# Kernel optimization log

Hardware: AMD Instinct MI355X
Metric: run time of the kernel (lower is better)

## Reference

```python
import jax, jax.numpy as jnp
import numpy as np

B, N, S, K = 8, 4096, 256, 128   # clouds, points/cloud, FPS samples (num_vote_test), neighbor cap
R = 0.2                           # ball-query radius
M = 45                            # FoldingNet grid side -> 45*45 = 2025 grid points


def _fps(pos):
    """Deterministic farthest point sampling of S points from pos [N,3] (start at index 0)."""
    n = pos.shape[0]
    big = jnp.finfo(pos.dtype).max

    def step(carry, _):
        mind, last = carry
        d = jnp.sum((pos - pos[last]) ** 2, axis=-1)
        mind = jnp.minimum(mind, d)
        nxt = jnp.argmax(mind).astype(jnp.int32)
        return (mind, nxt), nxt

    init = (jnp.full((n,), big, pos.dtype), jnp.int32(0))
    _, rest = jax.lax.scan(step, init, None, length=S - 1)
    return jnp.concatenate([jnp.zeros((1,), jnp.int32), rest])


def _forward(pos, Wt, bt, Wc1, bc1, Wc2, bc2, Wc3, bc3, We1, be1, We2, be2,
             Wf11, bf11, Wf12, bf12, Wf13, bf13, Wf21, bf21, Wf22, bf22, Wf23, bf23):
    lrelu = jax.nn.leaky_relu  # slope 0.01, matches torch LeakyReLU default
    # transformer: mlp([3,64]) -- BatchNorm at eval with default stats is identity
    x = lrelu(pos @ Wt + bt)                                  # [B,N,64]
    # FPS per cloud
    idx = jax.vmap(_fps)(pos)                                  # [B,S]
    new_pos = jnp.take_along_axis(pos, idx[..., None], axis=1)  # [B,S,3]
    # radius ball query: first K in-ball neighbors by index order (torch_cluster semantics)
    d2 = jnp.sum((new_pos[:, :, None, :] - pos[:, None, :, :]) ** 2, -1)  # [B,S,N]
    inball = d2 <= R * R
    keep = inball & (jnp.cumsum(inball, axis=-1) <= K)
    order = jnp.where(keep, jnp.arange(N)[None, None, :], N)
    nidx = jnp.sort(order, axis=-1)[..., :K]                   # [B,S,K]
    valid = nidx < N
    nsafe = jnp.minimum(nidx, N - 1)
    gather = jax.vmap(lambda a, i: a[i])
    xj = gather(x, nsafe)                                      # [B,S,K,64]
    pj = gather(pos, nsafe)                                    # [B,S,K,3]
    # PointConv: mlp(cat[x_j, pos_j - pos_i]) with max aggregation
    feat = jnp.concatenate([xj, pj - new_pos[:, :, None, :]], -1)  # [B,S,K,67]
    h = lrelu(feat @ Wc1 + bc1)
    h = lrelu(h @ Wc2 + bc2)
    h = lrelu(h @ Wc3 + bc3)                                   # [B,S,K,512]
    neg = jnp.finfo(h.dtype).min
    agg = jnp.max(jnp.where(valid[..., None], h, neg), axis=2)  # [B,S,512]
    # encoder mlp([515, 512, 2*bottleneck], last=True)
    e = lrelu(jnp.concatenate([agg, new_pos], -1) @ We1 + be1)
    e = e @ We2 + be2                                          # [B,S,2*bottleneck]
    mean, logvar = jnp.split(e, 2, axis=-1)
    std = jnp.exp(0.5 * logvar)
    # feature_selection (eval, rand=False): all S votes contribute; vote aggregation
    z = jnp.sum(mean / std, axis=1) / jnp.sum(1.0 / std, axis=1)  # [B,bottleneck]
    # FoldingNet decoder: 45x45 grid in [-0.3,0.3]^2, conv1x1 == last-dim linear
    g1 = np.linspace(-0.3, 0.3, M, dtype=np.float32)
    mg = np.meshgrid(g1, g1)
    grid = jnp.asarray(np.stack([mg[0].reshape(-1), mg[1].reshape(-1)], -1))  # [M*M,2]
    G = M * M
    code = jnp.broadcast_to(z[:, None, :], (z.shape[0], G, z.shape[1]))
    gb = jnp.broadcast_to(grid[None], (z.shape[0], G, 2))
    f = jnp.concatenate([code, gb], -1)                        # [B,G,bottleneck+2]
    f = jax.nn.relu(f @ Wf11 + bf11)
    f = jax.nn.relu(f @ Wf12 + bf12)
    f = f @ Wf13 + bf13                                        # [B,G,3]
    f2 = jnp.concatenate([code, f], -1)                        # [B,G,bottleneck+3]
    f2 = jax.nn.relu(f2 @ Wf21 + bf21)
    f2 = jax.nn.relu(f2 @ Wf22 + bf22)
    return f2 @ Wf23 + bf23                                    # [B,G,3]


_PARAM_SHAPES = [
    ("Wt", (3, 64)), ("bt", (64,)),
    ("Wc1", (67, 64)), ("bc1", (64,)),
    ("Wc2", (64, 128)), ("bc2", (128,)),
    ("Wc3", (128, 512)), ("bc3", (512,)),
    ("We1", (515, 512)), ("be1", (512,)),
    ("We2", (512, 2048)), ("be2", (2048,)),
    ("Wf11", (1026, 512)), ("bf11", (512,)),
    ("Wf12", (512, 512)), ("bf12", (512,)),
    ("Wf13", (512, 3)), ("bf13", (3,)),
    ("Wf21", (1027, 512)), ("bf21", (512,)),
    ("Wf22", (512, 512)), ("bf22", (512,)),
    ("Wf23", (512, 3)), ("bf23", (3,)),
]


def setup_inputs() -> dict:
    key = jax.random.key(0)
    inp = {"pos": jax.random.uniform(key, (B, N, 3), jnp.float32)}
    for i, (nm, sh) in enumerate(_PARAM_SHAPES):
        k = jax.random.fold_in(key, i + 1)
        fan_in = sh[0]
        inp[nm] = jax.random.normal(k, sh, jnp.float32) / np.sqrt(fan_in)
    return inp


def reference(pos, Wt, bt, Wc1, bc1, Wc2, bc2, Wc3, bc3, We1, be1, We2, be2,
              Wf11, bf11, Wf12, bf12, Wf13, bf13, Wf21, bf21, Wf22, bf22, Wf23, bf23):
    return _forward(pos, Wt, bt, Wc1, bc1, Wc2, bc2, Wc3, bc3, We1, be1, We2, be2,
                    Wf11, bf11, Wf12, bf12, Wf13, bf13, Wf21, bf21, Wf22, bf22, Wf23, bf23)
```

## Files before the change

### kernel.cpp

```cpp
#include <hip/hip_runtime.h>
#include <math.h>

#define BATCH 8
#define NPTS 4096
#define SSAMP 256
#define KNBR 128
#define GGRID 2025

typedef __attribute__((ext_vector_type(8))) short bf16x8;
typedef __attribute__((ext_vector_type(8))) unsigned short u16x8;
typedef __attribute__((ext_vector_type(4))) float f32x4;
#define MFMA16(a, b, c) __builtin_amdgcn_mfma_f32_16x16x32_bf16((a), (b), (c), 0, 0, 0)

__device__ __forceinline__ float lrelu01(float v) { return v > 0.f ? v : 0.01f * v; }
__device__ __forceinline__ unsigned short f2bf(float f) {
    unsigned u = __float_as_uint(f);
    unsigned r = (u + 0x7FFFu + ((u >> 16) & 1u)) >> 16;
    return (unsigned short)r;
}
__device__ __forceinline__ unsigned long long umax64(unsigned long long a, unsigned long long b) {
    return a > b ? a : b;
}
__device__ __forceinline__ void spin_ge(const int* p, int target) {
    while (__hip_atomic_load(p, __ATOMIC_RELAXED, __HIP_MEMORY_SCOPE_AGENT) < target)
        __builtin_amdgcn_s_sleep(16);
}
__device__ __forceinline__ float aload(const float* p) {
    return __hip_atomic_load((float*)p, __ATOMIC_RELAXED, __HIP_MEMORY_SCOPE_AGENT);
}
__device__ __forceinline__ void astore(float* p, float v) {
    __hip_atomic_store(p, v, __ATOMIC_RELAXED, __HIP_MEMORY_SCOPE_AGENT);
}

__global__ void preconv_kernel(const float* __restrict__ Wc1, const float* __restrict__ Wc2,
                               const float* __restrict__ Wc3, const float* __restrict__ We1,
                               const float* __restrict__ We2, const float* __restrict__ Wf12,
                               const float* __restrict__ Wf22,
                               unsigned short* __restrict__ W1T, unsigned short* __restrict__ W2T,
                               unsigned short* __restrict__ W3T, unsigned short* __restrict__ We1T,
                               unsigned short* __restrict__ We2T, unsigned short* __restrict__ Wf12T,
                               unsigned short* __restrict__ Wf22T) {
    int o = blockIdx.x * 256 + threadIdx.x;
    const int S1 = 6144, S2 = 8192, S3 = 65536, S4 = 294912, S5 = 1048576, S6 = 262144;
    if (o < S1) { int n = o / 96, k = o - n * 96; W1T[o] = f2bf(k < 67 ? Wc1[k * 64 + n] : 0.f); return; }
    o -= S1;
    if (o < S2) { int n = o >> 6, k = o & 63; W2T[o] = f2bf(Wc2[k * 128 + n]); return; }
    o -= S2;
    if (o < S3) { int n = o >> 7, k = o & 127; W3T[o] = f2bf(Wc3[k * 512 + n]); return; }
    o -= S3;
    if (o < S4) { int n = o / 576, k = o - n * 576; We1T[o] = f2bf(k < 515 ? We1[k * 512 + n] : 0.f); return; }
    o -= S4;
    if (o < S5) {
        int np = o >> 9, k = o & 511;
        int src = (np & 1) ? 1024 + (np >> 1) : (np >> 1);
        We2T[o] = f2bf(We2[(size_t)k * 2048 + src]);
        return;
    }
    o -= S5;
    if (o < S6) { int n = o >> 9, k = o & 511; Wf12T[o] = f2bf(Wf12[k * 512 + n]); return; }
    o -= S6;
    { int n = o >> 9, k = o & 511; Wf22T[o] = f2bf(Wf22[k * 512 + n]); }
}

__global__ void __launch_bounds__(256, 3) stage1_kernel(
    const float* __restrict__ pos, float* __restrict__ newpos, int* __restrict__ prog,
    const float* __restrict__ Wt, const float* __restrict__ bt,
    const unsigned short* __restrict__ W1T, const unsigned short* __restrict__ W2T,
    const unsigned short* __restrict__ W3T,
    const float* __restrict__ bc1, const float* __restrict__ bc2, const float* __restrict__ bc3,
    unsigned short* __restrict__ encin) {
    __shared__ __align__(16) unsigned char smem[53760];
    int blk = blockIdx.x, t = threadIdx.x;
    int wave = t >> 6, lane = t & 63;

    if (blk < 8) {
        float* pxs = (float*)smem;
        float* pys = (float*)(smem + 16384);
        float* pzs = (float*)(smem + 32768);
        float* npb = (float*)(smem + 49152);
        unsigned long long* rk = (unsigned long long*)(smem + 52224);
        int b = blk;
        const float* P = pos + (size_t)b * NPTS * 3;
        float* np = newpos + (size_t)b * SSAMP * 3;
        float px[16], py[16], pz[16], mind[16];
#pragma unroll
        for (int j = 0; j < 16; ++j) {
            int n = t + 256 * j;
            float X = P[n * 3 + 0], Y = P[n * 3 + 1], Z = P[n * 3 + 2];
            px[j] = X; py[j] = Y; pz[j] = Z;
            pxs[n] = X; pys[n] = Y; pzs[n] = Z;
            mind[j] = 3.402823466e+38f;
        }
        float cx = P[0], cy = P[1], cz = P[2];
        if (t == 0) { npb[0] = cx; npb[1] = cy; npb[2] = cz; }
        __syncthreads();
        for (int s = 1; s < SSAMP; ++s) {
            int p = s & 1;
            unsigned long long k[16];
#pragma unroll
            for (int j = 0; j < 16; ++j) {
                float dx = __fsub_rn(px[j], cx), dy = __fsub_rn(py[j], cy), dz = __fsub_rn(pz[j], cz);
                float d = __fadd_rn(__fadd_rn(__fmul_rn(dx, dx), __fmul_rn(dy, dy)), __fmul_rn(dz, dz));
                mind[j] = fminf(mind[j], d);
                k[j] = ((unsigned long long)__float_as_uint(mind[j]) << 32)
                     | (unsigned)~(unsigned)(t + 256 * j);
            }
#pragma unroll
            for (int st = 8; st > 0; st >>= 1)
#pragma unroll
                for (int j = 0; j < st; ++j) k[j] = umax64(k[j], k[j + st]);
            unsigned long long key = k[0];
            {
                unsigned long long a = __shfl_xor(key, 1, 64);
                unsigned long long b2 = __shfl_xor(key, 2, 64);
                unsigned long long c = __shfl_xor(key, 3, 64);
                key = umax64(umax64(key, a), umax64(b2, c));
                a = __shfl_xor(key, 4, 64);
                b2 = __shfl_xor(key, 8, 64);
                c = __shfl_xor(key, 12, 64);
                key = umax64(umax64(key, a), umax64(b2, c));
                a = __shfl_xor(key, 16, 64);
                b2 = __shfl_xor(key, 32, 64);
                c = __shfl_xor(key, 48, 64);
                key = umax64(umax64(key, a), umax64(b2, c));
            }
            if (lane == 0) rk[p * 4 + wave] = key;
            __syncthreads();
            unsigned long long k0 = rk[p * 4 + 0], k1 = rk[p * 4 + 1];
            unsigned long long k2 = rk[p * 4 + 2], k3 = rk[p * 4 + 3];
            unsigned long long bk = umax64(umax64(k0, k1), umax64(k2, k3));
            int nx = (int)(~(unsigned)(bk & 0xFFFFFFFFull));
            cx = pxs[nx]; cy = pys[nx]; cz = pzs[nx];
            if (t == 0) {
                npb[s * 3 + 0] = cx;
                npb[s * 3 + 1] = cy;
                npb[s * 3 + 2] = cz;
            }
            if ((s & 7) == 7) {
                if (t < 24) astore(&np[(s - 7) * 3 + t], npb[(s - 7) * 3 + t]);
                if (t == 0 && s >= 15)
                    __hip_atomic_store(&prog[b], s - 8, __ATOMIC_RELAXED, __HIP_MEMORY_SCOPE_AGENT);
            }
        }
        __syncthreads();
        if (t == 0)
            __hip_atomic_store(&prog[b], 255, __ATOMIC_RELAXED, __HIP_MEMORY_SCOPE_AGENT);
        return;
    }

    unsigned short* featl = (unsigned short*)smem;
    unsigned short* h2    = (unsigned short*)smem;
    unsigned short* h1    = (unsigned short*)(smem + 34816);
    float* mred = (float*)(smem + 34816);
    int*   vld  = (int*)(smem + 53248);
    int*   wl   = (int*)smem;
    int*   cnt  = (int*)(smem + 2048);
    float* wtb  = (float*)(smem + 26624);

    int cons = blk - 8;
    int s = cons >> 3, b = cons & 7;
    int bs = b * 256 + s;
    int quad = lane >> 4, l16 = lane & 15;

    if (t == 0) spin_ge(&prog[b], s);
    __syncthreads();
    float q0 = aload(&newpos[(size_t)bs * 3 + 0]);
    float q1 = aload(&newpos[(size_t)bs * 3 + 1]);
    float q2 = aload(&newpos[(size_t)bs * 3 + 2]);

    const float* P = pos + (size_t)b * NPTS * 3;
    {
        int base = 0;
        for (int c = 0; c < 16 && base < KNBR; ++c) {
            int n = wave * 1024 + c * 64 + lane;
            float dx = __fsub_rn(P[n * 3 + 0], q0);
            float dy = __fsub_rn(P[n * 3 + 1], q1);
            float dz = __fsub_rn(P[n * 3 + 2], q2);
            float d2 = __fadd_rn(__fadd_rn(__fmul_rn(dx, dx), __fmul_rn(dy, dy)), __fmul_rn(dz, dz));
            bool in = (d2 <= 0.04f);
            unsigned long long mask = __ballot(in);
            if (in) {
                int p = base + __popcll(mask & ((1ull << lane) - 1ull));
                if (p < KNBR) wl[wave * 128 + p] = n;
            }
            base += __popcll(mask);
        }
        if (lane == 0) cnt[wave] = base < KNBR ? base : KNBR;
    }
    __syncthreads();
    {
        int c0 = cnt[0], c1 = cnt[1], c2 = cnt[2], c3 = cnt[3];
        if (t < 128) {
            int idx = -1, r = t;
            if (r < c0) idx = wl[r];
            else {
                r -= c0;
                if (r < c1) idx = wl[128 + r];
                else {
                    r -= c1;
                    if (r < c2) idx = wl[256 + r];
                    else { r -= c2; if (r < c3) idx = wl[384 + r]; }
                }
            }
            vld[t] = idx;
        }
        if (t < 192) wtb[t] = Wt[t];
        else wtb[t] = bt[t - 192];
    }
    __syncthreads();

    int vbits = 0;
#pragma unroll
    for (int i = 0; i < 2; ++i)
#pragma unroll
        for (int reg = 0; reg < 4; ++reg)
            if (vld[(2 * wave + i) * 16 + quad * 4 + reg] >= 0) vbits |= 1 << (i * 4 + reg);

    {
        int sr = t >> 1, sh = t & 1;
        int n = vld[sr];
        int ns = n < 0 ? 0 : n;
        const float* pp = pos + ((size_t)b * NPTS + ns) * 3;
        float p0 = pp[0], p1 = pp[1], p2 = pp[2];
        unsigned short* frow = &featl[sr * 104];
        u16x8 z8 = {0, 0, 0, 0, 0, 0, 0, 0};
        if (n >= 0) {
#pragma unroll
            for (int g = 0; g < 4; ++g) {
                u16x8 v8;
#pragma unroll
                for (int e = 0; e < 8; ++e) {
                    int c = sh * 32 + g * 8 + e;
                    float v = fmaf(p2, wtb[128 + c], fmaf(p1, wtb[64 + c], fmaf(p0, wtb[c], wtb[192 + c])));
                    v8[e] = (unsigned short)f2bf(lrelu01(v));
                }
                *(u16x8*)&frow[sh * 32 + g * 8] = v8;
            }
        } else {
#pragma unroll
            for (int g = 0; g < 4; ++g) *(u16x8*)&frow[sh * 32 + g * 8] = z8;
        }
        if (sh == 1) {
            u16x8 dv = z8;
            if (n >= 0) {
                dv[0] = (unsigned short)f2bf(__fsub_rn(p0, q0));
                dv[1] = (unsigned short)f2bf(__fsub_rn(p1, q1));
                dv[2] = (unsigned short)f2bf(__fsub_rn(p2, q2));
            }
            *(u16x8*)&frow[64] = dv;
            *(u16x8*)&frow[72] = z8;
            *(u16x8*)&frow[80] = z8;
            *(u16x8*)&frow[88] = z8;
        }
    }
    __syncthreads();

    {
        f32x4 acc[2][4];
#pragma unroll
        for (int i = 0; i < 2; ++i)
#pragma unroll
            for (int nt = 0; nt < 4; ++nt) acc[i][nt] = (f32x4){0.f, 0.f, 0.f, 0.f};
#pragma unroll
        for (int ks = 0; ks < 3; ++ks) {
            bf16x8 afr[2];
#pragma unroll
            for (int i = 0; i < 2; ++i)
                afr[i] = *(const bf16x8*)&featl[((2 * wave + i) * 16 + l16) * 104 + ks * 32 + quad * 8];
#pragma unroll
            for (int nt = 0; nt < 4; ++nt) {
                bf16x8 bfr = *(const bf16x8*)(W1T + (nt * 16 + l16) * 96 + ks * 32 + quad * 8);
                acc[0][nt] = MFMA16(afr[0], bfr, acc[0][nt]);
                acc[1][nt] = MFMA16(afr[1], bfr, acc[1][nt]);
            }
        }
#pragma unroll
        for (int i = 0; i < 2; ++i)
#pragma unroll
            for (int nt = 0; nt < 4; ++nt) {
                int col = nt * 16 + l16;
                float bias = bc1[col];
#pragma unroll
                for (int reg = 0; reg < 4; ++reg) {
                    int row = (2 * wave + i) * 16 + quad * 4 + reg;
                    h1[row * 72 + col] = f2bf(lrelu01(acc[i][nt][reg] + bias));
                }
            }
    }
    __syncthreads();

    {
        f32x4 acc[2][8];
#pragma unroll
        for (int i = 0; i < 2; ++i)
#pragma unroll
            for (int nt = 0; nt < 8; ++nt) acc[i][nt] = (f32x4){0.f, 0.f, 0.f, 0.f};
#pragma unroll
        for (int ks = 0; ks < 2; ++ks) {
            bf16x8 afr[2];
#pragma unroll
            for (int i = 0; i < 2; ++i)
                afr[i] = *(const bf16x8*)&h1[((2 * wave + i) * 16 + l16) * 72 + ks * 32 + quad * 8];
#pragma unroll
            for (int nt = 0; nt < 8; ++nt) {
                bf16x8 bfr = *(const bf16x8*)(W2T + (nt * 16 + l16) * 64 + ks * 32 + quad * 8);
                acc[0][nt] = MFMA16(afr[0], bfr, acc[0][nt]);
                acc[1][nt] = MFMA16(afr[1], bfr, acc[1][nt]);
            }
        }
        __syncthreads();
#pragma unroll
        for (int i = 0; i < 2; ++i)
#pragma unroll
            for (int nt = 0; nt < 8; ++nt) {
                int col = nt * 16 + l16;
                float bias = bc2[col];
#pragma unroll
                for (int reg = 0; reg < 4; ++reg) {
                    int row = (2 * wave + i) * 16 + quad * 4 + reg;
                    h2[row * 136 + col] = f2bf(lrelu01(acc[i][nt][reg] + bias));
                }
            }
    }
    __syncthreads();

    for (int c3 = 0; c3 < 4; ++c3) {
        f32x4 acc[2][8];
#pragma unroll
        for (int i = 0; i < 2; ++i)
#pragma unroll
            for (int nt = 0; nt < 8; ++nt) acc[i][nt] = (f32x4){0.f, 0.f, 0.f, 0.f};
#pragma unroll
        for (int ks = 0; ks < 4; ++ks) {
            bf16x8 afr[2];
#pragma unroll
            for (int i = 0; i < 2; ++i)
                afr[i] = *(const bf16x8*)&h2[((2 * wave + i) * 16 + l16) * 136 + ks * 32 + quad * 8];
#pragma unroll
            for (int nt = 0; nt < 8; ++nt) {
                bf16x8 bfr = *(const bf16x8*)(W3T + ((size_t)((c3 * 8 + nt) * 16 + l16)) * 128 + ks * 32 + quad * 8);
                acc[0][nt] = MFMA16(afr[0], bfr, acc[0][nt]);
                acc[1][nt] = MFMA16(afr[1], bfr, acc[1][nt]);
            }
        }
#pragma unroll
        for (int nt = 0; nt < 8; ++nt) {
            float vmax = -3.402823466e+38f;
#pragma unroll
            for (int i = 0; i < 2; ++i)
#pragma unroll
                for (int reg = 0; reg < 4; ++reg)
                    if (vbits & (1 << (i * 4 + reg))) vmax = fmaxf(vmax, acc[i][nt][reg]);
            vmax = fmaxf(vmax, __shfl_xor(vmax, 16));
            vmax = fmaxf(vmax, __shfl_xor(vmax, 32));
            if (lane < 16) mred[wave * 512 + (c3 * 8 + nt) * 16 + l16] = vmax;
        }
    }
    __syncthreads();
    unsigned short* erow = encin + (size_t)bs * 576;
    for (int c = t; c < 576; c += 256) {
        unsigned short v;
        if (c < 512) {
            float m4 = fmaxf(fmaxf(mred[c], mred[512 + c]), fmaxf(mred[1024 + c], mred[1536 + c]));
            v = f2bf(lrelu01(m4 + bc3[c]));
        } else if (c < 515) {
            v = f2bf(c == 512 ? q0 : (c == 513 ? q1 : q2));
        } else v = 0;
        erow[c] = v;
    }
}

__global__ void __launch_bounds__(256, 2) tail_kernel(
    const unsigned short* __restrict__ encinh, const unsigned short* __restrict__ We1T,
    const float* __restrict__ be1, unsigned short* __restrict__ e1h,
    const unsigned short* __restrict__ We2T, const float* __restrict__ be2,
    float* __restrict__ zacc, int* __restrict__ cnts,
    const float* __restrict__ Wf11, const float* __restrict__ bf11,
    const float* __restrict__ Wf21, const float* __restrict__ bf21,
    float* __restrict__ u1, float* __restrict__ u2,
    const unsigned short* __restrict__ Wf12T, const float* __restrict__ bf12,
    const float* __restrict__ Wf13, const float* __restrict__ bf13,
    const unsigned short* __restrict__ Wf22T, const float* __restrict__ bf22,
    const float* __restrict__ Wf23, const float* __restrict__ bf23,
    float* __restrict__ pts, float* __restrict__ outv) {
    __shared__ __align__(16) unsigned char smem[40960];
    int blk = blockIdx.x, t = threadIdx.x;
    int wave = t >> 6, lane = t & 63, quad = lane >> 4, l16 = lane & 15;

    if (blk < 320) {
        unsigned short* As = (unsigned short*)smem;
        bool is_e1 = blk < 64;
        int rb, cb;
        const unsigned short* A;
        const unsigned short* BT;
        int Ka;
        if (is_e1) { rb = blk >> 2; cb = blk & 3; A = encinh; BT = We1T; Ka = 576; }
        else {
            int j = blk - 64; rb = j >> 4; cb = j & 15; A = e1h; BT = We2T; Ka = 512;
            if (t == 0) spin_ge(&cnts[rb], 4);
            __syncthreads();
            __threadfence();
        }
        int row0 = rb * 128, col0 = cb * 128;
        f32x4 acc[2][8];
#pragma unroll
        for (int i = 0; i < 2; ++i)
#pragma unroll
            for (int nt = 0; nt < 8; ++nt) acc[i][nt] = (f32x4){0.f, 0.f, 0.f, 0.f};
        int nk = Ka >> 6;
        int sr = t >> 1, sh = t & 1;
        const unsigned short* Arow = A + (size_t)(row0 + sr) * Ka + sh * 32;
        for (int ks = 0; ks < nk; ++ks) {
            u16x8 av[4];
#pragma unroll
            for (int j = 0; j < 4; ++j) av[j] = *(const u16x8*)(Arow + ks * 64 + j * 8);
            __syncthreads();
#pragma unroll
            for (int j = 0; j < 4; ++j) *(u16x8*)&As[sr * 72 + sh * 32 + j * 8] = av[j];
            __syncthreads();
#pragma unroll
            for (int ks2 = 0; ks2 < 2; ++ks2) {
                bf16x8 afr0 = *(const bf16x8*)&As[((2 * wave) * 16 + l16) * 72 + ks2 * 32 + quad * 8];
                bf16x8 afr1 = *(const bf16x8*)&As[((2 * wave + 1) * 16 + l16) * 72 + ks2 * 32 + quad * 8];
#pragma unroll
                for (int nt = 0; nt < 8; ++nt) {
                    bf16x8 bfr = *(const bf16x8*)(BT + (size_t)(col0 + nt * 16 + l16) * Ka + ks * 64 + ks2 * 32 + quad * 8);
                    acc[0][nt] = MFMA16(afr0, bfr, acc[0][nt]);
                    acc[1][nt] = MFMA16(afr1, bfr, acc[1][nt]);
                }
            }
        }
        if (is_e1) {
#pragma unroll
            for (int i = 0; i < 2; ++i)
#pragma unroll
                for (int nt = 0; nt < 8; ++nt) {
                    int col = col0 + nt * 16 + l16;
                    float bv = be1[col];
#pragma unroll
                    for (int reg = 0; reg < 4; ++reg) {
                        int row = row0 + (2 * wave + i) * 16 + quad * 4 + reg;
                        e1h[(size_t)row * 512 + col] = f2bf(lrelu01(acc[i][nt][reg] + bv));
                    }
                }
            __syncthreads();
            if (t == 0) { __threadfence(); atomicAdd(&cnts[rb], 1); }
        } else {
            int b = row0 >> 8;
#pragma unroll
            for (int nt = 0; nt < 8; ++nt) {
                int colp = col0 + nt * 16 + l16;
                int c2 = colp >> 1;
                int srcc = (colp & 1) ? 1024 + c2 : c2;
                float bv = be2[srcc];
                float num = 0.f, den = 0.f;
#pragma unroll
                for (int i = 0; i < 2; ++i)
#pragma unroll
                    for (int reg = 0; reg < 4; ++reg) {
                        float val = acc[i][nt][reg] + bv;
                        float par = __shfl_xor(val, 1, 64);
                        float d = expf(-0.5f * par);
                        num += val * d;
                        den += d;
                    }
                num += __shfl_xor(num, 16, 64); den += __shfl_xor(den, 16, 64);
                num += __shfl_xor(num, 32, 64); den += __shfl_xor(den, 32, 64);
                if (quad == 0 && !(l16 & 1)) {
                    atomicAdd(&zacc[((b << 10) + c2) * 2 + 0], num);
                    atomicAdd(&zacc[((b << 10) + c2) * 2 + 1], den);
                }
            }
            __syncthreads();
            if (t == 0) atomicAdd(&cnts[16], 1);
        }
        return;
    }

    if (blk < 336) {
        float* zt = (float*)smem;
        float* red = (float*)(smem + 32768);
        int j = blk - 320;
        int dec = j >> 3, cb = j & 7;
        const float* W = dec ? Wf21 : Wf11;
        const float* bias = dec ? bf21 : bf11;
        float* u = dec ? u2 : u1;
        if (t == 0) spin_ge(&cnts[16], 256);
        __syncthreads();
#pragma unroll
        for (int i = 0; i < 32; ++i) {
            int o = t + i * 256;
            float num = aload(&zacc[o * 2 + 0]);
            float den = aload(&zacc[o * 2 + 1]);
            zt[(o & 1023) * 8 + (o >> 10)] = num / den;
        }
        __syncthreads();
        int c64 = t & 63, kc = t >> 6;
        int co = cb * 64 + c64;
        float acc[8];
#pragma unroll
        for (int r = 0; r < 8; ++r) acc[r] = 0.f;
        for (int i = 0; i < 256; ++i) {
            int ci = kc * 256 + i;
            float w = W[(size_t)ci * 512 + co];
            const float4* zp = (const float4*)&zt[ci * 8];
            float4 z0 = zp[0], z1 = zp[1];
            acc[0] = fmaf(z0.x, w, acc[0]); acc[1] = fmaf(z0.y, w, acc[1]);
            acc[2] = fmaf(z0.z, w, acc[2]); acc[3] = fmaf(z0.w, w, acc[3]);
            acc[4] = fmaf(z1.x, w, acc[4]); acc[5] = fmaf(z1.y, w, acc[5]);
            acc[6] = fmaf(z1.z, w, acc[6]); acc[7] = fmaf(z1.w, w, acc[7]);
        }
#pragma unroll
        for (int r = 0; r < 8; ++r) red[(kc * 64 + c64) * 8 + r] = acc[r];
        __syncthreads();
        if (kc == 0) {
#pragma unroll
            for (int r = 0; r < 8; ++r) {
                float v = red[(0 * 64 + c64) * 8 + r] + red[(1 * 64 + c64) * 8 + r]
                        + red[(2 * 64 + c64) * 8 + r] + red[(3 * 64 + c64) * 8 + r] + bias[co];
                astore(&u[r * 512 + co], v);
            }
        }
        __syncthreads();
        if (t == 0) atomicAdd(&cnts[17 + dec], 1);
        return;
    }

    {
        unsigned short* As = (unsigned short*)smem;
        float* sW = (float*)(smem + 18432);
        float* sU = (float*)(smem + 24576);
        float* sP = (float*)(smem + 28672);
        float* sB = (float*)(smem + 30208);
        float* sRC = (float*)(smem + 30720);
        int dec = blk < 844 ? 0 : 1;
        int idx0 = blk - (dec ? 844 : 336);
        int j = idx0 >> 2, cc = idx0 & 3;
        const float* u = dec ? u2 : u1;
        const float* Wfold = dec ? Wf21 : Wf11;
        int nExtra = dec ? 3 : 2;
        const unsigned short* WT = dec ? Wf22T : Wf12T;
        const float* bmid = dec ? bf22 : bf12;
        const float* wout = dec ? Wf23 : Wf13;
        const float* bout = dec ? bf23 : bf13;
        float* ov = dec ? outv : pts;
        int row0 = j * 128, col0 = cc * 128;
        int b0 = row0 / 2025;

        for (int idx = t; idx < 1536; idx += 256) {
            int r = idx >> 9, c = idx & 511;
            sW[r * 512 + c] = (r < nExtra) ? Wfold[(size_t)(1024 + r) * 512 + c] : 0.f;
        }
        for (int idx = t; idx < 384; idx += 256) sP[idx] = wout[col0 * 3 + idx];
        if (t < 128) sB[t] = bmid[col0 + t];
        if (dec == 0 && t < 128) {
            int rg = row0 + t; if (rg > 16199) rg = 16199;
            int b = rg / 2025, g = rg - b * 2025;
            int i = g / 45, jj = g - i * 45;
            sRC[t * 4 + 0] = (jj == 44) ? 0.3f : (float)(-0.3 + jj * (0.6 / 44.0));
            sRC[t * 4 + 1] = (i == 44) ? 0.3f : (float)(-0.3 + i * (0.6 / 44.0));
            sRC[t * 4 + 2] = 0.f;
            sRC[t * 4 + 3] = __int_as_float(b - b0);
        }

        if (t == 0) {
            spin_ge(&cnts[17 + dec], 8);
            if (dec) spin_ge(&cnts[20 + j], 4);
        }
        __syncthreads();

        for (int idx = t; idx < 1024; idx += 256) {
            int rb = idx >> 9;
            int bb = b0 + rb; if (bb > 7) bb = 7;
            sU[rb * 512 + (idx & 511)] = aload(&u[bb * 512 + (idx & 511)]);
        }
        if (dec == 1 && t < 128) {
            int rg = row0 + t; if (rg > 16199) rg = 16199;
            int b = rg / 2025;
            sRC[t * 4 + 0] = aload(&pts[rg * 3 + 0]);
            sRC[t * 4 + 1] = aload(&pts[rg * 3 + 1]);
            sRC[t * 4 + 2] = aload(&pts[rg * 3 + 2]);
            sRC[t * 4 + 3] = __int_as_float(b - b0);
        }
        __syncthreads();

        float proj[2][4][3];
#pragma unroll
        for (int i = 0; i < 2; ++i)
#pragma unroll
            for (int r = 0; r < 4; ++r) { proj[i][r][0] = 0.f; proj[i][r][1] = 0.f; proj[i][r][2] = 0.f; }

        int sr = t >> 1, sh = t & 1;
        float4 rc = *(const float4*)&sRC[sr * 4];
        int ubi = __float_as_int(rc.w);
        const float* up = sU + ubi * 512;
        f32x4 acc[2][8];
#pragma unroll
        for (int i = 0; i < 2; ++i)
#pragma unroll
            for (int nt = 0; nt < 8; ++nt) acc[i][nt] = (f32x4){0.f, 0.f, 0.f, 0.f};
        for (int ks = 0; ks < 8; ++ks) {
            __syncthreads();
            {
                int cbase = ks * 64 + sh * 32;
                const float4* w0p = (const float4*)&sW[cbase];
                const float4* w1p = (const float4*)&sW[512 + cbase];
                const float4* w2p = (const float4*)&sW[1024 + cbase];
                const float4* uup = (const float4*)&up[cbase];
#pragma unroll
                for (int g4 = 0; g4 < 8; ++g4) {
                    float4 w0 = w0p[g4], w1 = w1p[g4], w2 = w2p[g4], uu = uup[g4];
                    float v0 = fmaf(rc.z, w2.x, fmaf(rc.y, w1.x, fmaf(rc.x, w0.x, uu.x)));
                    float v1 = fmaf(rc.z, w2.y, fmaf(rc.y, w1.y, fmaf(rc.x, w0.y, uu.y)));
                    float v2 = fmaf(rc.z, w2.z, fmaf(rc.y, w1.z, fmaf(rc.x, w0.z, uu.z)));
                    float v3 = fmaf(rc.z, w2.w, fmaf(rc.y, w1.w, fmaf(rc.x, w0.w, uu.w)));
                    uint2 pk;
                    pk.x = (unsigned)f2bf(fmaxf(v0, 0.f)) | ((unsigned)f2bf(fmaxf(v1, 0.f)) << 16);
                    pk.y = (unsigned)f2bf(fmaxf(v2, 0.f)) | ((unsigned)f2bf(fmaxf(v3, 0.f)) << 16);
                    *(uint2*)&As[sr * 72 + sh * 32 + g4 * 4] = pk;
                }
            }
            __syncthreads();
#pragma unroll
            for (int ks2 = 0; ks2 < 2; ++ks2) {
                bf16x8 afr0 = *(const bf16x8*)&As[((2 * wave) * 16 + l16) * 72 + ks2 * 32 + quad * 8];
                bf16x8 afr1 = *(const bf16x8*)&As[((2 * wave + 1) * 16 + l16) * 72 + ks2 * 32 + quad * 8];
#pragma unroll
                for (int nt = 0; nt < 8; ++nt) {
                    bf16x8 bfr = *(const bf16x8*)(WT + (size_t)(col0 + nt * 16 + l16) * 512 + ks * 64 + ks2 * 32 + quad * 8);
                    acc[0][nt] = MFMA16(afr0, bfr, acc[0][nt]);
                    acc[1][nt] = MFMA16(afr1, bfr, acc[1][nt]);
                }
            }
        }
#pragma unroll
        for (int i = 0; i < 2; ++i)
#pragma unroll
            for (int nt = 0; nt < 8; ++nt) {
                int lc = nt * 16 + l16;
                float bv = sB[lc];
                float w0 = sP[lc * 3 + 0], w1 = sP[lc * 3 + 1], w2 = sP[lc * 3 + 2];
#pragma unroll
                for (int reg = 0; reg < 4; ++reg) {
                    float h = fmaxf(acc[i][nt][reg] + bv, 0.f);
                    proj[i][reg][0] = fmaf(h, w0, proj[i][reg][0]);
                    proj[i][reg][1] = fmaf(h, w1, proj[i][reg][1]);
                    proj[i][reg][2] = fmaf(h, w2, proj[i][reg][2]);
                }
            }
        float o0 = (cc == 0) ? bout[0] : 0.f;
        float o1 = (cc == 0) ? bout[1] : 0.f;
        float o2 = (cc == 0) ? bout[2] : 0.f;
#pragma unroll
        for (int i = 0; i < 2; ++i)
#pragma unroll
            for (int reg = 0; reg < 4; ++reg) {
                float p0 = proj[i][reg][0], p1 = proj[i][reg][1], p2 = proj[i][reg][2];
#pragma unroll
                for (int m = 1; m < 16; m <<= 1) {
                    p0 += __shfl_xor(p0, m, 64);
                    p1 += __shfl_xor(p1, m, 64);
                    p2 += __shfl_xor(p2, m, 64);
                }
                if (l16 == 0) {
                    int row = row0 + (2 * wave + i) * 16 + quad * 4 + reg;
                    if (row < 16200) {
                        atomicAdd(&ov[row * 3 + 0], p0 + o0);
                        atomicAdd(&ov[row * 3 + 1], p1 + o1);
                        atomicAdd(&ov[row * 3 + 2], p2 + o2);
                    }
                }
            }
        if (dec == 0) {
            __syncthreads();
            if (t == 0) atomicAdd(&cnts[20 + j], 1);
        }
    }
}

extern "C" void kernel_launch(void* const* d_in, const int* in_sizes, int n_in,
                              void* d_out, int out_size, void* d_ws, size_t ws_size,
                              hipStream_t stream) {
    const float* pos  = (const float*)d_in[0];
    const float* Wt   = (const float*)d_in[1];
    const float* bt   = (const float*)d_in[2];
    const float* Wc1  = (const float*)d_in[3];
    const float* bc1  = (const float*)d_in[4];
    const float* Wc2  = (const float*)d_in[5];
    const float* bc2  = (const float*)d_in[6];
    const float* Wc3  = (const float*)d_in[7];
    const float* bc3  = (const float*)d_in[8];
    const float* We1  = (const float*)d_in[9];
    const float* be1  = (const float*)d_in[10];
    const float* We2  = (const float*)d_in[11];
    const float* be2  = (const float*)d_in[12];
    const float* Wf11 = (const float*)d_in[13];
    const float* bf11 = (const float*)d_in[14];
    const float* Wf12 = (const float*)d_in[15];
    const float* bf12 = (const float*)d_in[16];
    const float* Wf13 = (const float*)d_in[17];
    const float* bf13 = (const float*)d_in[18];
    const float* Wf21 = (const float*)d_in[19];
    const float* bf21 = (const float*)d_in[20];
    const float* Wf22 = (const float*)d_in[21];
    const float* bf22 = (const float*)d_in[22];
    const float* Wf23 = (const float*)d_in[23];
    const float* bf23 = (const float*)d_in[24];
    float* out = (float*)d_out;

    float* wsf = (float*)d_ws;
    size_t off = 0;
    unsigned short* encinh= (unsigned short*)(wsf + off); off += 589824;
    unsigned short* e1h   = (unsigned short*)(wsf + off); off += 524288;
    float* zacc = wsf + off; off += 16384;
    float* u1   = wsf + off; off += 4096;
    float* u2   = wsf + off; off += 4096;
    float* pts  = wsf + off; off += 48600;
    float* newp = wsf + off; off += 6144;
    int*   prog = (int*)(wsf + off); off += 16;
    int*   cnts = (int*)(wsf + off); off += 256;
    unsigned short* W1T   = (unsigned short*)(wsf + off); off += 3072;
    unsigned short* W2T   = (unsigned short*)(wsf + off); off += 4096;
    unsigned short* W3T   = (unsigned short*)(wsf + off); off += 32768;
    unsigned short* We1T  = (unsigned short*)(wsf + off); off += 147456;
    unsigned short* We2T  = (unsigned short*)(wsf + off); off += 524288;
    unsigned short* Wf12T = (unsigned short*)(wsf + off); off += 131072;
    unsigned short* Wf22T = (unsigned short*)(wsf + off); off += 131072;

    hipMemsetAsync(prog, 0xFF, 64, stream);
    hipMemsetAsync(cnts, 0x00, 1024, stream);
    hipMemsetAsync(zacc, 0x00, 16384 * 4, stream);
    hipMemsetAsync(pts, 0x00, 48600 * 4, stream);
    hipMemsetAsync(out, 0x00, (size_t)out_size * 4, stream);
    preconv_kernel<<<7608, 256, 0, stream>>>(Wc1, Wc2, Wc3, We1, We2, Wf12, Wf22,
                                             W1T, W2T, W3T, We1T, We2T, Wf12T, Wf22T);
    stage1_kernel<<<2056, 256, 0, stream>>>(pos, newp, prog, Wt, bt, W1T, W2T, W3T,
                                            bc1, bc2, bc3, encinh);
    tail_kernel<<<1352, 256, 0, stream>>>(encinh, We1T, be1, e1h, We2T, be2, zacc, cnts,
                                          Wf11, bf11, Wf21, bf21, u1, u2,
                                          Wf12T, bf12, Wf13, bf13,
                                          Wf22T, bf22, Wf23, bf23, pts, out);
}
```

Before: 590.0 us.

## Move encoder and u-projection stages from tail kernel into stage1 persistent kernel

Extends stage1 with an extra 336 blocks that run the encoder MLPs (We1, We2) and the folding u1/u2 projections, synchronized through counters, instead of running them in the tail kernel. The tail kernel keeps only the folding decoder blocks. The goal is to overlap encoder work with the FPS/PointConv stage and shorten the tail kernel, at the cost of more spin-wait dependencies and a risk of deadlock if the producer blocks are not scheduled.

```diff
diff --git a/kernel.cpp b/kernel.cpp
--- a/kernel.cpp
+++ b/kernel.cpp
@@ -64,14 +64,23 @@
 
 __global__ void __launch_bounds__(256, 3) stage1_kernel(
     const float* __restrict__ pos, float* __restrict__ newpos, int* __restrict__ prog,
+    int* __restrict__ cnts,
     const float* __restrict__ Wt, const float* __restrict__ bt,
     const unsigned short* __restrict__ W1T, const unsigned short* __restrict__ W2T,
     const unsigned short* __restrict__ W3T,
     const float* __restrict__ bc1, const float* __restrict__ bc2, const float* __restrict__ bc3,
-    unsigned short* __restrict__ encin) {
+    unsigned short* __restrict__ encin,
+    const unsigned short* __restrict__ We1T, const float* __restrict__ be1,
+    unsigned short* __restrict__ e1h,
+    const unsigned short* __restrict__ We2T, const float* __restrict__ be2,
+    float* __restrict__ zacc,
+    const float* __restrict__ Wf11, const float* __restrict__ bf11,
+    const float* __restrict__ Wf21, const float* __restrict__ bf21,
+    float* __restrict__ u1, float* __restrict__ u2) {
     __shared__ __align__(16) unsigned char smem[53760];
     int blk = blockIdx.x, t = threadIdx.x;
     int wave = t >> 6, lane = t & 63;
+    int quad = lane >> 4, l16 = lane & 15;
 
     if (blk < 8) {
         float* pxs = (float*)smem;
@@ -148,259 +157,247 @@
         return;
     }
 
-    unsigned short* featl = (unsigned short*)smem;
-    unsigned short* h2    = (unsigned short*)smem;
-    unsigned short* h1    = (unsigned short*)(smem + 34816);
-    float* mred = (float*)(smem + 34816);
-    int*   vld  = (int*)(smem + 53248);
-    int*   wl   = (int*)smem;
-    int*   cnt  = (int*)(smem + 2048);
-    float* wtb  = (float*)(smem + 26624);
-
-    int cons = blk - 8;
-    int s = cons >> 3, b = cons & 7;
-    int bs = b * 256 + s;
-    int quad = lane >> 4, l16 = lane & 15;
-
-    if (t == 0) spin_ge(&prog[b], s);
-    __syncthreads();
-    float q0 = aload(&newpos[(size_t)bs * 3 + 0]);
-    float q1 = aload(&newpos[(size_t)bs * 3 + 1]);
-    float q2 = aload(&newpos[(size_t)bs * 3 + 2]);
-
-    const float* P = pos + (size_t)b * NPTS * 3;
-    {
-        int base = 0;
-        for (int c = 0; c < 16 && base < KNBR; ++c) {
-            int n = wave * 1024 + c * 64 + lane;
-            float dx = __fsub_rn(P[n * 3 + 0], q0);
-            float dy = __fsub_rn(P[n * 3 + 1], q1);
-            float dz = __fsub_rn(P[n * 3 + 2], q2);
-            float d2 = __fadd_rn(__fadd_rn(__fmul_rn(dx, dx), __fmul_rn(dy, dy)), __fmul_rn(dz, dz));
-            bool in = (d2 <= 0.04f);
-            unsigned long long mask = __ballot(in);
-            if (in) {
-                int p = base + __popcll(mask & ((1ull << lane) - 1ull));
-                if (p < KNBR) wl[wave * 128 + p] = n;
-            }
-            base += __popcll(mask);
-        }
-        if (lane == 0) cnt[wave] = base < KNBR ? base : KNBR;
-    }
-    __syncthreads();
-    {
-        int c0 = cnt[0], c1 = cnt[1], c2 = cnt[2], c3 = cnt[3];
-        if (t < 128) {
-            int idx = -1, r = t;
-            if (r < c0) idx = wl[r];
-            else {
-                r -= c0;
-                if (r < c1) idx = wl[128 + r];
+    if (blk < 2056) {
+        unsigned short* featl = (unsigned short*)smem;
+        unsigned short* h2    = (unsigned short*)smem;
+        unsigned short* h1    = (unsigned short*)(smem + 34816);
+        float* mred = (float*)(smem + 34816);
+        int*   vld  = (int*)(smem + 53248);
+        int*   wl   = (int*)smem;
+        int*   cnt  = (int*)(smem + 2048);
+        float* wtb  = (float*)(smem + 26624);
+
+        int cons = blk - 8;
+        int s = cons >> 3, b = cons & 7;
+        int bs = b * 256 + s;
+
+        if (t == 0) spin_ge(&prog[b], s);
+        __syncthreads();
+        float q0 = aload(&newpos[(size_t)bs * 3 + 0]);
+        float q1 = aload(&newpos[(size_t)bs * 3 + 1]);
+        float q2 = aload(&newpos[(size_t)bs * 3 + 2]);
+
+        const float* P = pos + (size_t)b * NPTS * 3;
+        {
+            int base = 0;
+            for (int c = 0; c < 16 && base < KNBR; ++c) {
+                int n = wave * 1024 + c * 64 + lane;
+                float dx = __fsub_rn(P[n * 3 + 0], q0);
+                float dy = __fsub_rn(P[n * 3 + 1], q1);
+                float dz = __fsub_rn(P[n * 3 + 2], q2);
+                float d2 = __fadd_rn(__fadd_rn(__fmul_rn(dx, dx), __fmul_rn(dy, dy)), __fmul_rn(dz, dz));
+                bool in = (d2 <= 0.04f);
+                unsigned long long mask = __ballot(in);
+                if (in) {
+                    int p = base + __popcll(mask & ((1ull << lane) - 1ull));
+                    if (p < KNBR) wl[wave * 128 + p] = n;
+                }
+                base += __popcll(mask);
+            }
+            if (lane == 0) cnt[wave] = base < KNBR ? base : KNBR;
+        }
+        __syncthreads();
+        {
+            int c0 = cnt[0], c1 = cnt[1], c2 = cnt[2], c3 = cnt[3];
+            if (t < 128) {
+                int idx = -1, r = t;
+                if (r < c0) idx = wl[r];
                 else {
-                    r -= c1;
-                    if (r < c2) idx = wl[256 + r];
-                    else { r -= c2; if (r < c3) idx = wl[384 + r]; }
-                }
-            }
-            vld[t] = idx;
-        }
-        if (t < 192) wtb[t] = Wt[t];
-        else wtb[t] = bt[t - 192];
-    }
-    __syncthreads();
-
-    int vbits = 0;
-#pragma unroll
-    for (int i = 0; i < 2; ++i)
-#pragma unroll
-        for (int reg = 0; reg < 4; ++reg)
-            if (vld[(2 * wave + i) * 16 + quad * 4 + reg] >= 0) vbits |= 1 << (i * 4 + reg);
-
-    {
-        int sr = t >> 1, sh = t & 1;
-        int n = vld[sr];
-        int ns = n < 0 ? 0 : n;
-        const float* pp = pos + ((size_t)b * NPTS + ns) * 3;
-        float p0 = pp[0], p1 = pp[1], p2 = pp[2];
-        unsigned short* frow = &featl[sr * 104];
-        u16x8 z8 = {0, 0, 0, 0, 0, 0, 0, 0};
-        if (n >= 0) {
-#pragma unroll
-            for (int g = 0; g < 4; ++g) {
-                u16x8 v8;
-#pragma unroll
-                for (int e = 0; e < 8; ++e) {
-                    int c = sh * 32 + g * 8 + e;
-                    float v = fmaf(p2, wtb[128 + c], fmaf(p1, wtb[64 + c], fmaf(p0, wtb[c], wtb[192 + c])));
-                    v8[e] = (unsigned short)f2bf(lrelu01(v));
-                }
-                *(u16x8*)&frow[sh * 32 + g * 8] = v8;
-            }
-        } else {
-#pragma unroll
-            for (int g = 0; g < 4; ++g) *(u16x8*)&frow[sh * 32 + g * 8] = z8;
-        }
-        if (sh == 1) {
-            u16x8 dv = z8;
+                    r -= c0;
+                    if (r < c1) idx = wl[128 + r];
+                    else {
+                        r -= c1;
+                        if (r < c2) idx = wl[256 + r];
+                        else { r -= c2; if (r < c3) idx = wl[384 + r]; }
+                    }
+                }
+                vld[t] = idx;
+            }
+            if (t < 192) wtb[t] = Wt[t];
+            else wtb[t] = bt[t - 192];
+        }
+        __syncthreads();
+
+        int vbits = 0;
+#pragma unroll
+        for (int i = 0; i < 2; ++i)
+#pragma unroll
+            for (int reg = 0; reg < 4; ++reg)
+                if (vld[(2 * wave + i) * 16 + quad * 4 + reg] >= 0) vbits |= 1 << (i * 4 + reg);
+
+        {
+            int sr = t >> 1, sh = t & 1;
+            int n = vld[sr];
+            int ns = n < 0 ? 0 : n;
+            const float* pp = pos + ((size_t)b * NPTS + ns) * 3;
+            float p0 = pp[0], p1 = pp[1], p2 = pp[2];
+            unsigned short* frow = &featl[sr * 104];
+            u16x8 z8 = {0, 0, 0, 0, 0, 0, 0, 0};
             if (n >= 0) {
-                dv[0] = (unsigned short)f2bf(__fsub_rn(p0, q0));
-                dv[1] = (unsigned short)f2bf(__fsub_rn(p1, q1));
-                dv[2] = (unsigned short)f2bf(__fsub_rn(p2, q2));
-            }
-            *(u16x8*)&frow[64] = dv;
-            *(u16x8*)&frow[72] = z8;
-            *(u16x8*)&frow[80] = z8;
-            *(u16x8*)&frow[88] = z8;
-        }
-    }
-    __syncthreads();
-
-    {
-        f32x4 acc[2][4];
-#pragma unroll
-        for (int i = 0; i < 2; ++i)
-#pragma unroll
-            for (int nt = 0; nt < 4; ++nt) acc[i][nt] = (f32x4){0.f, 0.f, 0.f, 0.f};
-#pragma unroll
-        for (int ks = 0; ks < 3; ++ks) {
-            bf16x8 afr[2];
+#pragma unroll
+                for (int g = 0; g < 4; ++g) {
+                    u16x8 v8;
+#pragma unroll
+                    for (int e = 0; e < 8; ++e) {
+                        int c = sh * 32 + g * 8 + e;
+                        float v = fmaf(p2, wtb[128 + c], fmaf(p1, wtb[64 + c], fmaf(p0, wtb[c], wtb[192 + c])));
+                        v8[e] = (unsigned short)f2bf(lrelu01(v));
+                    }
+                    *(u16x8*)&frow[sh * 32 + g * 8] = v8;
+                }
+            } else {
+#pragma unroll
+                for (int g = 0; g < 4; ++g) *(u16x8*)&frow[sh * 32 + g * 8] = z8;
+            }
+            if (sh == 1) {
+                u16x8 dv = z8;
+                if (n >= 0) {
+                    dv[0] = (unsigned short)f2bf(__fsub_rn(p0, q0));
+                    dv[1] = (unsigned short)f2bf(__fsub_rn(p1, q1));
+                    dv[2] = (unsigned short)f2bf(__fsub_rn(p2, q2));
+                }
+                *(u16x8*)&frow[64] = dv;
+                *(u16x8*)&frow[72] = z8;
+                *(u16x8*)&frow[80] = z8;
+                *(u16x8*)&frow[88] = z8;
+            }
+        }
+        __syncthreads();
+
+        {
+            f32x4 acc[2][4];
 #pragma unroll
             for (int i = 0; i < 2; ++i)
-                afr[i] = *(const bf16x8*)&featl[((2 * wave + i) * 16 + l16) * 104 + ks * 32 + quad * 8];
-#pragma unroll
-            for (int nt = 0; nt < 4; ++nt) {
-                bf16x8 bfr = *(const bf16x8*)(W1T + (nt * 16 + l16) * 96 + ks * 32 + quad * 8);
-                acc[0][nt] = MFMA16(afr[0], bfr, acc[0][nt]);
-                acc[1][nt] = MFMA16(afr[1], bfr, acc[1][nt]);
-            }
-        }
-#pragma unroll
-        for (int i = 0; i < 2; ++i)
-#pragma unroll
-            for (int nt = 0; nt < 4; ++nt) {
-                int col = nt * 16 + l16;
-                float bias = bc1[col];
-#pragma unroll
-                for (int reg = 0; reg < 4; ++reg) {
-                    int row = (2 * wave + i) * 16 + quad * 4 + reg;
-                    h1[row * 72 + col] = f2bf(lrelu01(acc[i][nt][reg] + bias));
-                }
-            }
-    }
-    __syncthreads();
-
-    {
-        f32x4 acc[2][8];
-#pragma unroll
-        for (int i = 0; i < 2; ++i)
-#pragma unroll
-            for (int nt = 0; nt < 8; ++nt) acc[i][nt] = (f32x4){0.f, 0.f, 0.f, 0.f};
-#pragma unroll
-        for (int ks = 0; ks < 2; ++ks) {
-            bf16x8 afr[2];
+#pragma unroll
+                for (int nt = 0; nt < 4; ++nt) acc[i][nt] = (f32x4){0.f, 0.f, 0.f, 0.f};
+#pragma unroll
+            for (int ks = 0; ks < 3; ++ks) {
+                bf16x8 afr[2];
+#pragma unroll
+                for (int i = 0; i < 2; ++i)
+                    afr[i] = *(const bf16x8*)&featl[((2 * wave + i) * 16 + l16) * 104 + ks * 32 + quad * 8];
+#pragma unroll
+                for (int nt = 0; nt < 4; ++nt) {
+                    bf16x8 bfr = *(const bf16x8*)(W1T + (nt * 16 + l16) * 96 + ks * 32 + quad * 8);
+                    acc[0][nt] = MFMA16(afr[0], bfr, acc[0][nt]);
+                    acc[1][nt] = MFMA16(afr[1], bfr, acc[1][nt]);
+                }
+            }
 #pragma unroll
             for (int i = 0; i < 2; ++i)
-                afr[i] = *(const bf16x8*)&h1[((2 * wave + i) * 16 + l16) * 72 + ks * 32 + quad * 8];
+#pragma unroll
+                for (int nt = 0; nt < 4; ++nt) {
+                    int col = nt * 16 + l16;
+                    float bias = bc1[col];
+#pragma unroll
+                    for (int reg = 0; reg < 4; ++reg) {
+                        int row = (2 * wave + i) * 16 + quad * 4 + reg;
+                        h1[row * 72 + col] = f2bf(lrelu01(acc[i][nt][reg] + bias));
+                    }
+                }
+        }
+        __syncthreads();
+
+        {
+            f32x4 acc[2][8];
+#pragma unroll
+            for (int i = 0; i < 2; ++i)
+#pragma unroll
+                for (int nt = 0; nt < 8; ++nt) acc[i][nt] = (f32x4){0.f, 0.f, 0.f, 0.f};
+#pragma unroll
+            for (int ks = 0; ks < 2; ++ks) {
+                bf16x8 afr[2];
+#pragma unroll
+                for (int i = 0; i < 2; ++i)
+                    afr[i] = *(const bf16x8*)&h1[((2 * wave + i) * 16 + l16) * 72 + ks * 32 + quad * 8];
+#pragma unroll
+                for (int nt = 0; nt < 8; ++nt) {
+                    bf16x8 bfr = *(const bf16x8*)(W2T + (nt * 16 + l16) * 64 + ks * 32 + quad * 8);
+                    acc[0][nt] = MFMA16(afr[0], bfr, acc[0][nt]);
+                    acc[1][nt] = MFMA16(afr[1], bfr, acc[1][nt]);
+                }
+            }
+            __syncthreads();
+#pragma unroll
+            for (int i = 0; i < 2; ++i)
+#pragma unroll
+                for (int nt = 0; nt < 8; ++nt) {
+                    int col = nt * 16 + l16;
+                    float bias = bc2[col];
+#pragma unroll
+                    for (int reg = 0; reg < 4; ++reg) {
+                        int row = (2 * wave + i) * 16 + quad * 4 + reg;
+                        h2[row * 136 + col] = f2bf(lrelu01(acc[i][nt][reg] + bias));
+                    }
+                }
+        }
+        __syncthreads();
+
+        for (int c3 = 0; c3 < 4; ++c3) {
+            f32x4 acc[2][8];
+#pragma unroll
+            for (int i = 0; i < 2; ++i)
+#pragma unroll
+                for (int nt = 0; nt < 8; ++nt) acc[i][nt] = (f32x4){0.f, 0.f, 0.f, 0.f};
+#pragma unroll
+            for (int ks = 0; ks < 4; ++ks) {
+                bf16x8 afr[2];
+#pragma unroll
+                for (int i = 0; i < 2; ++i)
+                    afr[i] = *(const bf16x8*)&h2[((2 * wave + i) * 16 + l16) * 136 + ks * 32 + quad * 8];
+#pragma unroll
+                for (int nt = 0; nt < 8; ++nt) {
+                    bf16x8 bfr = *(const bf16x8*)(W3T + ((size_t)((c3 * 8 + nt) * 16 + l16)) * 128 + ks * 32 + quad * 8);
+                    acc[0][nt] = MFMA16(afr[0], bfr, acc[0][nt]);
+                    acc[1][nt] = MFMA16(afr[1], bfr, acc[1][nt]);
+                }
+            }
 #pragma unroll
             for (int nt = 0; nt < 8; ++nt) {
-                bf16x8 bfr = *(const bf16x8*)(W2T + (nt * 16 + l16) * 64 + ks * 32 + quad * 8);
-                acc[0][nt] = MFMA16(afr[0], bfr, acc[0][nt]);
-                acc[1][nt] = MFMA16(afr[1], bfr, acc[1][nt]);
-            }
-        }
-        __syncthreads();
-#pragma unroll
-        for (int i = 0; i < 2; ++i)
-#pragma unroll
-            for (int nt = 0; nt < 8; ++nt) {
-                int col = nt * 16 + l16;
-                float bias = bc2[col];
-#pragma unroll
-                for (int reg = 0; reg < 4; ++reg) {
-                    int row = (2 * wave + i) * 16 + quad * 4 + reg;
-                    h2[row * 136 + col] = f2bf(lrelu01(acc[i][nt][reg] + bias));
-                }
-            }
-    }
-    __syncthreads();
-
-    for (int c3 = 0; c3 < 4; ++c3) {
-        f32x4 acc[2][8];
-#pragma unroll
-        for (int i = 0; i < 2; ++i)
-#pragma unroll
-            for (int nt = 0; nt < 8; ++nt) acc[i][nt] = (f32x4){0.f, 0.f, 0.f, 0.f};
-#pragma unroll
-        for (int ks = 0; ks < 4; ++ks) {
-            bf16x8 afr[2];
-#pragma unroll
-            for (int i = 0; i < 2; ++i)
-                afr[i] = *(const bf16x8*)&h2[((2 * wave + i) * 16 + l16) * 136 + ks * 32 + quad * 8];
-#pragma unroll
-            for (int nt = 0; nt < 8; ++nt) {
-                bf16x8 bfr = *(const bf16x8*)(W3T + ((size_t)((c3 * 8 + nt) * 16 + l16)) * 128 + ks * 32 + quad * 8);
-                acc[0][nt] = MFMA16(afr[0], bfr, acc[0][nt]);
-                acc[1][nt] = MFMA16(afr[1], bfr, acc[1][nt]);
-            }
-        }
-#pragma unroll
-        for (int nt = 0; nt < 8; ++nt) {
-            float vmax = -3.402823466e+38f;
-#pragma unroll
-            for (int i = 0; i < 2; ++i)
-#pragma unroll
-                for (int reg = 0; reg < 4; ++reg)
-                    if (vbits & (1 << (i * 4 + reg))) vmax = fmaxf(vmax, acc[i][nt][reg]);
-            vmax = fmaxf(vmax, __shfl_xor(vmax, 16));
-            vmax = fmaxf(vmax, __shfl_xor(vmax, 32));
-            if (lane < 16) mred[wave * 512 + (c3 * 8 + nt) * 16 + l16] = vmax;
-        }
-    }
-    __syncthreads();
-    unsigned short* erow = encin + (size_t)bs * 576;
-    for (int c = t; c < 576; c += 256) {
-        unsigned short v;
-        if (c < 512) {
-            float m4 = fmaxf(fmaxf(mred[c], mred[512 + c]), fmaxf(mred[1024 + c], mred[1536 + c]));
-            v = f2bf(lrelu01(m4 + bc3[c]));
-        } else if (c < 515) {
-            v = f2bf(c == 512 ? q0 : (c == 513 ? q1 : q2));
-        } else v = 0;
-        erow[c] = v;
-    }
-}
-
-__global__ void __launch_bounds__(256, 2) tail_kernel(
-    const unsigned short* __restrict__ encinh, const unsigned short* __restrict__ We1T,
-    const float* __restrict__ be1, unsigned short* __restrict__ e1h,
-    const unsigned short* __restrict__ We2T, const float* __restrict__ be2,
-    float* __restrict__ zacc, int* __restrict__ cnts,
-    const float* __restrict__ Wf11, const float* __restrict__ bf11,
-    const float* __restrict__ Wf21, const float* __restrict__ bf21,
-    float* __restrict__ u1, float* __restrict__ u2,
-    const unsigned short* __restrict__ Wf12T, const float* __restrict__ bf12,
-    const float* __restrict__ Wf13, const float* __restrict__ bf13,
-    const unsigned short* __restrict__ Wf22T, const float* __restrict__ bf22,
-    const float* __restrict__ Wf23, const float* __restrict__ bf23,
-    float* __restrict__ pts, float* __restrict__ outv) {
-    __shared__ __align__(16) unsigned char smem[40960];
-    int blk = blockIdx.x, t = threadIdx.x;
-    int wave = t >> 6, lane = t & 63, quad = lane >> 4, l16 = lane & 15;
-
-    if (blk < 320) {
+                float vmax = -3.402823466e+38f;
+#pragma unroll
+                for (int i = 0; i < 2; ++i)
+#pragma unroll
+                    for (int reg = 0; reg < 4; ++reg)
+                        if (vbits & (1 << (i * 4 + reg))) vmax = fmaxf(vmax, acc[i][nt][reg]);
+                vmax = fmaxf(vmax, __shfl_xor(vmax, 16));
+                vmax = fmaxf(vmax, __shfl_xor(vmax, 32));
+                if (lane < 16) mred[wave * 512 + (c3 * 8 + nt) * 16 + l16] = vmax;
+            }
+        }
+        __syncthreads();
+        unsigned short* erow = encin + (size_t)bs * 576;
+        for (int c = t; c < 576; c += 256) {
+            unsigned short v;
+            if (c < 512) {
+                float m4 = fmaxf(fmaxf(mred[c], mred[512 + c]), fmaxf(mred[1024 + c], mred[1536 + c]));
+                v = f2bf(lrelu01(m4 + bc3[c]));
+            } else if (c < 515) {
+                v = f2bf(c == 512 ? q0 : (c == 513 ? q1 : q2));
+            } else v = 0;
+            erow[c] = v;
+        }
+        __syncthreads();
+        if (t == 0) { __threadfence(); atomicAdd(&cnts[150 + (bs >> 7)], 1); }
+        return;
+    }
+
+    if (blk < 2376) {
         unsigned short* As = (unsigned short*)smem;
-        bool is_e1 = blk < 64;
+        bool is_e1 = blk < 2120;
         int rb, cb;
         const unsigned short* A;
         const unsigned short* BT;
         int Ka;
-        if (is_e1) { rb = blk >> 2; cb = blk & 3; A = encinh; BT = We1T; Ka = 576; }
-        else {
-            int j = blk - 64; rb = j >> 4; cb = j & 15; A = e1h; BT = We2T; Ka = 512;
+        if (is_e1) {
+            int j = blk - 2056; rb = j >> 2; cb = j & 3; A = encin; BT = We1T; Ka = 576;
+            if (t == 0) spin_ge(&cnts[150 + rb], 128);
+        } else {
+            int j = blk - 2120; rb = j >> 4; cb = j & 15; A = e1h; BT = We2T; Ka = 512;
             if (t == 0) spin_ge(&cnts[rb], 4);
-            __syncthreads();
-            __threadfence();
-        }
+        }
+        __syncthreads();
+        __threadfence();
         int row0 = rb * 128, col0 = cb * 128;
         f32x4 acc[2][8];
 #pragma unroll
@@ -413,10 +410,10 @@
         for (int ks = 0; ks < nk; ++ks) {
             u16x8 av[4];
 #pragma unroll
-            for (int j = 0; j < 4; ++j) av[j] = *(const u16x8*)(Arow + ks * 64 + j * 8);
+            for (int j2 = 0; j2 < 4; ++j2) av[j2] = *(const u16x8*)(Arow + ks * 64 + j2 * 8);
             __syncthreads();
 #pragma unroll
-            for (int j = 0; j < 4; ++j) *(u16x8*)&As[sr * 72 + sh * 32 + j * 8] = av[j];
+            for (int j2 = 0; j2 < 4; ++j2) *(u16x8*)&As[sr * 72 + sh * 32 + j2 * 8] = av[j2];
             __syncthreads();
 #pragma unroll
             for (int ks2 = 0; ks2 < 2; ++ks2) {
@@ -477,10 +474,10 @@
         return;
     }
 
-    if (blk < 336) {
+    {
         float* zt = (float*)smem;
         float* red = (float*)(smem + 32768);
-        int j = blk - 320;
+        int j = blk - 2376;
         int dec = j >> 3, cb = j & 7;
         const float* W = dec ? Wf21 : Wf11;
         const float* bias = dec ? bf21 : bf11;
@@ -521,60 +518,67 @@
                 astore(&u[r * 512 + co], v);
             }
         }
-        __syncthreads();
-        if (t == 0) atomicAdd(&cnts[17 + dec], 1);
-        return;
-    }
-
-    {
-        unsigned short* As = (unsigned short*)smem;
-        float* sW = (float*)(smem + 18432);
-        float* sU = (float*)(smem + 24576);
-        float* sP = (float*)(smem + 28672);
-        float* sB = (float*)(smem + 30208);
-        float* sRC = (float*)(smem + 30720);
-        int dec = blk < 844 ? 0 : 1;
-        int idx0 = blk - (dec ? 844 : 336);
-        int j = idx0 >> 2, cc = idx0 & 3;
-        const float* u = dec ? u2 : u1;
-        const float* Wfold = dec ? Wf21 : Wf11;
-        int nExtra = dec ? 3 : 2;
-        const unsigned short* WT = dec ? Wf22T : Wf12T;
-        const float* bmid = dec ? bf22 : bf12;
-        const float* wout = dec ? Wf23 : Wf13;
-        const float* bout = dec ? bf23 : bf13;
-        float* ov = dec ? outv : pts;
-        int row0 = j * 128, col0 = cc * 128;
-        int b0 = row0 / 2025;
-
-        for (int idx = t; idx < 1536; idx += 256) {
-            int r = idx >> 9, c = idx & 511;
-            sW[r * 512 + c] = (r < nExtra) ? Wfold[(size_t)(1024 + r) * 512 + c] : 0.f;
-        }
-        for (int idx = t; idx < 384; idx += 256) sP[idx] = wout[col0 * 3 + idx];
-        if (t < 128) sB[t] = bmid[col0 + t];
-        if (dec == 0 && t < 128) {
-            int rg = row0 + t; if (rg > 16199) rg = 16199;
-            int b = rg / 2025, g = rg - b * 2025;
-            int i = g / 45, jj = g - i * 45;
-            sRC[t * 4 + 0] = (jj == 44) ? 0.3f : (float)(-0.3 + jj * (0.6 / 44.0));
-            sRC[t * 4 + 1] = (i == 44) ? 0.3f : (float)(-0.3 + i * (0.6 / 44.0));
-            sRC[t * 4 + 2] = 0.f;
-            sRC[t * 4 + 3] = __int_as_float(b - b0);
-        }
-
-        if (t == 0) {
-            spin_ge(&cnts[17 + dec], 8);
-            if (dec) spin_ge(&cnts[20 + j], 4);
-        }
-        __syncthreads();
-
-        for (int idx = t; idx < 1024; idx += 256) {
-            int rb = idx >> 9;
-            int bb = b0 + rb; if (bb > 7) bb = 7;
-            sU[rb * 512 + (idx & 511)] = aload(&u[bb * 512 + (idx & 511)]);
-        }
-        if (dec == 1 && t < 128) {
+    }
+}
+
+__global__ void __launch_bounds__(256, 2) tail_kernel(
+    int* __restrict__ cnts,
+    const float* __restrict__ Wf11, const float* __restrict__ Wf21,
+    const float* __restrict__ u1, const float* __restrict__ u2,
+    const unsigned short* __restrict__ Wf12T, const float* __restrict__ bf12,
+    const float* __restrict__ Wf13, const float* __restrict__ bf13,
+    const unsigned short* __restrict__ Wf22T, const float* __restrict__ bf22,
+    const float* __restrict__ Wf23, const float* __restrict__ bf23,
+    float* __restrict__ pts, float* __restrict__ outv) {
+    __shared__ __align__(16) unsigned char smem[40960];
+    int blk = blockIdx.x, t = threadIdx.x;
+    int wave = t >> 6, lane = t & 63, quad = lane >> 4, l16 = lane & 15;
+
+    unsigned short* As = (unsigned short*)smem;
+    float* sW = (float*)(smem + 18432);
+    float* sU = (float*)(smem + 24576);
+    float* sP = (float*)(smem + 28672);
+    float* sB = (float*)(smem + 30208);
+    float* sRC = (float*)(smem + 30720);
+    int dec = blk < 508 ? 0 : 1;
+    int idx0 = blk - (dec ? 508 : 0);
+    int j = idx0 >> 2, cc = idx0 & 3;
+    const float* u = dec ? u2 : u1;
+    const float* Wfold = dec ? Wf21 : Wf11;
+    int nExtra = dec ? 3 : 2;
+    const unsigned short* WT = dec ? Wf22T : Wf12T;
+    const float* bmid = dec ? bf22 : bf12;
+    const float* wout = dec ? Wf23 : Wf13;
+    const float* bout = dec ? bf23 : bf13;
+    float* ov = dec ? outv : pts;
+    int row0 = j * 128, col0 = cc * 128;
+    int b0 = row0 / 2025;
+
+    for (int idx = t; idx < 1536; idx += 256) {
+        int r = idx >> 9, c = idx & 511;
+        sW[r * 512 + c] = (r < nExtra) ? Wfold[(size_t)(1024 + r) * 512 + c] : 0.f;
+    }
+    for (int idx = t; idx < 384; idx += 256) sP[idx] = wout[col0 * 3 + idx];
+    if (t < 128) sB[t] = bmid[col0 + t];
+    for (int idx = t; idx < 1024; idx += 256) {
+        int rb = idx >> 9;
+        int bb = b0 + rb; if (bb > 7) bb = 7;
+        sU[rb * 512 + (idx & 511)] = aload(&u[bb * 512 + (idx & 511)]);
+    }
+    if (dec == 0 && t < 128) {
+        int rg = row0 + t; if (rg > 16199) rg = 16199;
+        int b = rg / 2025, g = rg - b * 2025;
+        int i = g / 45, jj = g - i * 45;
+        sRC[t * 4 + 0] = (jj == 44) ? 0.3f : (float)(-0.3 + jj * (0.6 / 44.0));
+        sRC[t * 4 + 1] = (i == 44) ? 0.3f : (float)(-0.3 + i * (0.6 / 44.0));
+        sRC[t * 4 + 2] = 0.f;
+        sRC[t * 4 + 3] = __int_as_float(b - b0);
+    }
+
+    if (dec) {
+        if (t == 0) spin_ge(&cnts[20 + j], 4);
+        __syncthreads();
+        if (t < 128) {
             int rg = row0 + t; if (rg > 16199) rg = 16199;
             int b = rg / 2025;
             sRC[t * 4 + 0] = aload(&pts[rg * 3 + 0]);
@@ -582,99 +586,99 @@
             sRC[t * 4 + 2] = aload(&pts[rg * 3 + 2]);
             sRC[t * 4 + 3] = __int_as_float(b - b0);
         }
-        __syncthreads();
-
-        float proj[2][4][3];
-#pragma unroll
-        for (int i = 0; i < 2; ++i)
-#pragma unroll
-            for (int r = 0; r < 4; ++r) { proj[i][r][0] = 0.f; proj[i][r][1] = 0.f; proj[i][r][2] = 0.f; }
-
-        int sr = t >> 1, sh = t & 1;
-        float4 rc = *(const float4*)&sRC[sr * 4];
-        int ubi = __float_as_int(rc.w);
-        const float* up = sU + ubi * 512;
-        f32x4 acc[2][8];
-#pragma unroll
-        for (int i = 0; i < 2; ++i)
-#pragma unroll
-            for (int nt = 0; nt < 8; ++nt) acc[i][nt] = (f32x4){0.f, 0.f, 0.f, 0.f};
-        for (int ks = 0; ks < 8; ++ks) {
-            __syncthreads();
-            {
-                int cbase = ks * 64 + sh * 32;
-                const float4* w0p = (const float4*)&sW[cbase];
-                const float4* w1p = (const float4*)&sW[512 + cbase];
-                const float4* w2p = (const float4*)&sW[1024 + cbase];
-                const float4* uup = (const float4*)&up[cbase];
-#pragma unroll
-                for (int g4 = 0; g4 < 8; ++g4) {
-                    float4 w0 = w0p[g4], w1 = w1p[g4], w2 = w2p[g4], uu = uup[g4];
-                    float v0 = fmaf(rc.z, w2.x, fmaf(rc.y, w1.x, fmaf(rc.x, w0.x, uu.x)));
-                    float v1 = fmaf(rc.z, w2.y, fmaf(rc.y, w1.y, fmaf(rc.x, w0.y, uu.y)));
-                    float v2 = fmaf(rc.z, w2.z, fmaf(rc.y, w1.z, fmaf(rc.x, w0.z, uu.z)));
-                    float v3 = fmaf(rc.z, w2.w, fmaf(rc.y, w1.w, fmaf(rc.x, w0.w, uu.w)));
-                    uint2 pk;
-                    pk.x = (unsigned)f2bf(fmaxf(v0, 0.f)) | ((unsigned)f2bf(fmaxf(v1, 0.f)) << 16);
-                    pk.y = (unsigned)f2bf(fmaxf(v2, 0.f)) | ((unsigned)f2bf(fmaxf(v3, 0.f)) << 16);
-                    *(uint2*)&As[sr * 72 + sh * 32 + g4 * 4] = pk;
-                }
-            }
-            __syncthreads();
-#pragma unroll
-            for (int ks2 = 0; ks2 < 2; ++ks2) {
-                bf16x8 afr0 = *(const bf16x8*)&As[((2 * wave) * 16 + l16) * 72 + ks2 * 32 + quad * 8];
-                bf16x8 afr1 = *(const bf16x8*)&As[((2 * wave + 1) * 16 + l16) * 72 + ks2 * 32 + quad * 8];
-#pragma unroll
-                for (int nt = 0; nt < 8; ++nt) {
-                    bf16x8 bfr = *(const bf16x8*)(WT + (size_t)(col0 + nt * 16 + l16) * 512 + ks * 64 + ks2 * 32 + quad * 8);
-                    acc[0][nt] = MFMA16(afr0, bfr, acc[0][nt]);
-                    acc[1][nt] = MFMA16(afr1, bfr, acc[1][nt]);
-                }
-            }
-        }
-#pragma unroll
-        for (int i = 0; i < 2; ++i)
+    }
+    __syncthreads();
+
+    float proj[2][4][3];
+#pragma unroll
+    for (int i = 0; i < 2; ++i)
+#pragma unroll
+        for (int r = 0; r < 4; ++r) { proj[i][r][0] = 0.f; proj[i][r][1] = 0.f; proj[i][r][2] = 0.f; }
+
+    int sr = t >> 1, sh = t & 1;
+    float4 rc = *(const float4*)&sRC[sr * 4];
+    int ubi = __float_as_int(rc.w);
+    const float* up = sU + ubi * 512;
+    f32x4 acc[2][8];
+#pragma unroll
+    for (int i = 0; i < 2; ++i)
+#pragma unroll
+        for (int nt = 0; nt < 8; ++nt) acc[i][nt] = (f32x4){0.f, 0.f, 0.f, 0.f};
+    for (int ks = 0; ks < 8; ++ks) {
+        __syncthreads();
+        {
+            int cbase = ks * 64 + sh * 32;
+            const float4* w0p = (const float4*)&sW[cbase];
+            const float4* w1p = (const float4*)&sW[512 + cbase];
+            const float4* w2p = (const float4*)&sW[1024 + cbase];
+            const float4* uup = (const float4*)&up[cbase];
+#pragma unroll
+            for (int g4 = 0; g4 < 8; ++g4) {
+                float4 w0 = w0p[g4], w1 = w1p[g4], w2 = w2p[g4], uu = uup[g4];
+                float v0 = fmaf(rc.z, w2.x, fmaf(rc.y, w1.x, fmaf(rc.x, w0.x, uu.x)));
+                float v1 = fmaf(rc.z, w2.y, fmaf(rc.y, w1.y, fmaf(rc.x, w0.y, uu.y)));
+                float v2 = fmaf(rc.z, w2.z, fmaf(rc.y, w1.z, fmaf(rc.x, w0.z, uu.z)));
+                float v3 = fmaf(rc.z, w2.w, fmaf(rc.y, w1.w, fmaf(rc.x, w0.w, uu.w)));
+                uint2 pk;
+                pk.x = (unsigned)f2bf(fmaxf(v0, 0.f)) | ((unsigned)f2bf(fmaxf(v1, 0.f)) << 16);
+                pk.y = (unsigned)f2bf(fmaxf(v2, 0.f)) | ((unsigned)f2bf(fmaxf(v3, 0.f)) << 16);
+                *(uint2*)&As[sr * 72 + sh * 32 + g4 * 4] = pk;
+            }
+        }
+        __syncthreads();
+#pragma unroll
+        for (int ks2 = 0; ks2 < 2; ++ks2) {
+            bf16x8 afr0 = *(const bf16x8*)&As[((2 * wave) * 16 + l16) * 72 + ks2 * 32 + quad * 8];
+            bf16x8 afr1 = *(const bf16x8*)&As[((2 * wave + 1) * 16 + l16) * 72 + ks2 * 32 + quad * 8];
 #pragma unroll
             for (int nt = 0; nt < 8; ++nt) {
-                int lc = nt * 16 + l16;
-                float bv = sB[lc];
-                float w0 = sP[lc * 3 + 0], w1 = sP[lc * 3 + 1], w2 = sP[lc * 3 + 2];
-#pragma unroll
-                for (int reg = 0; reg < 4; ++reg) {
-                    float h = fmaxf(acc[i][nt][reg] + bv, 0.f);
-                    proj[i][reg][0] = fmaf(h, w0, proj[i][reg][0]);
-                    proj[i][reg][1] = fmaf(h, w1, proj[i][reg][1]);
-                    proj[i][reg][2] = fmaf(h, w2, proj[i][reg][2]);
-                }
-            }
-        float o0 = (cc == 0) ? bout[0] : 0.f;
-        float o1 = (cc == 0) ? bout[1] : 0.f;
-        float o2 = (cc == 0) ? bout[2] : 0.f;
-#pragma unroll
-        for (int i = 0; i < 2; ++i)
+                bf16x8 bfr = *(const bf16x8*)(WT + (size_t)(col0 + nt * 16 + l16) * 512 + ks * 64 + ks2 * 32 + quad * 8);
+                acc[0][nt] = MFMA16(afr0, bfr, acc[0][nt]);
+                acc[1][nt] = MFMA16(afr1, bfr, acc[1][nt]);
+            }
+        }
+    }
+#pragma unroll
+    for (int i = 0; i < 2; ++i)
+#pragma unroll
+        for (int nt = 0; nt < 8; ++nt) {
+            int lc = nt * 16 + l16;
+            float bv = sB[lc];
+            float w0 = sP[lc * 3 + 0], w1 = sP[lc * 3 + 1], w2 = sP[lc * 3 + 2];
 #pragma unroll
             for (int reg = 0; reg < 4; ++reg) {
-                float p0 = proj[i][reg][0], p1 = proj[i][reg][1], p2 = proj[i][reg][2];
-#pragma unroll
-                for (int m = 1; m < 16; m <<= 1) {
-                    p0 += __shfl_xor(p0, m, 64);
-                    p1 += __shfl_xor(p1, m, 64);
-                    p2 += __shfl_xor(p2, m, 64);
-                }
-                if (l16 == 0) {
-                    int row = row0 + (2 * wave + i) * 16 + quad * 4 + reg;
-                    if (row < 16200) {
-                        atomicAdd(&ov[row * 3 + 0], p0 + o0);
-                        atomicAdd(&ov[row * 3 + 1], p1 + o1);
-                        atomicAdd(&ov[row * 3 + 2], p2 + o2);
-                    }
-                }
-            }
-        if (dec == 0) {
-            __syncthreads();
-            if (t == 0) atomicAdd(&cnts[20 + j], 1);
-        }
+                float h = fmaxf(acc[i][nt][reg] + bv, 0.f);
+                proj[i][reg][0] = fmaf(h, w0, proj[i][reg][0]);
+                proj[i][reg][1] = fmaf(h, w1, proj[i][reg][1]);
+                proj[i][reg][2] = fmaf(h, w2, proj[i][reg][2]);
+            }
+        }
+    float o0 = (cc == 0) ? bout[0] : 0.f;
+    float o1 = (cc == 0) ? bout[1] : 0.f;
+    float o2 = (cc == 0) ? bout[2] : 0.f;
+#pragma unroll
+    for (int i = 0; i < 2; ++i)
+#pragma unroll
+        for (int reg = 0; reg < 4; ++reg) {
+            float p0 = proj[i][reg][0], p1 = proj[i][reg][1], p2 = proj[i][reg][2];
+#pragma unroll
+            for (int m = 1; m < 16; m <<= 1) {
+                p0 += __shfl_xor(p0, m, 64);
+                p1 += __shfl_xor(p1, m, 64);
+                p2 += __shfl_xor(p2, m, 64);
+            }
+            if (l16 == 0) {
+                int row = row0 + (2 * wave + i) * 16 + quad * 4 + reg;
+                if (row < 16200) {
+                    atomicAdd(&ov[row * 3 + 0], p0 + o0);
+                    atomicAdd(&ov[row * 3 + 1], p1 + o1);
+                    atomicAdd(&ov[row * 3 + 2], p2 + o2);
+                }
+            }
+        }
+    if (dec == 0) {
+        __syncthreads();
+        if (t == 0) atomicAdd(&cnts[20 + j], 1);
     }
 }
 
@@ -734,10 +738,11 @@
     hipMemsetAsync(out, 0x00, (size_t)out_size * 4, stream);
     preconv_kernel<<<7608, 256, 0, stream>>>(Wc1, Wc2, Wc3, We1, We2, Wf12, Wf22,
                                              W1T, W2T, W3T, We1T, We2T, Wf12T, Wf22T);
-    stage1_kernel<<<2056, 256, 0, stream>>>(pos, newp, prog, Wt, bt, W1T, W2T, W3T,
-                                            bc1, bc2, bc3, encinh);
-    tail_kernel<<<1352, 256, 0, stream>>>(encinh, We1T, be1, e1h, We2T, be2, zacc, cnts,
-                                          Wf11, bf11, Wf21, bf21, u1, u2,
+    stage1_kernel<<<2392, 256, 0, stream>>>(pos, newp, prog, cnts, Wt, bt, W1T, W2T, W3T,
+                                            bc1, bc2, bc3, encinh,
+                                            We1T, be1, e1h, We2T, be2, zacc,
+                                            Wf11, bf11, Wf21, bf21, u1, u2);
+    tail_kernel<<<1016, 256, 0, stream>>>(cnts, Wf11, Wf21, u1, u2,
                                           Wf12T, bf12, Wf13, bf13,
                                           Wf22T, bf22, Wf23, bf23, pts, out);
 }
```

Measured after the change: 588.6 us (median of 2 runs). About the same (-0.2%).
